# Optimization experiments

Measured on AMD Instinct MI355X. Metric: run time of the kernel, lower is better.

Reference implementation:

```python
import jax, jax.numpy as jnp
import numpy as np

UPDATE_RATE = 0.5
ALIVE_THRESH = 0.1

_SHIFTS = [(di, dj) for di in (-1, 0, 1) for dj in (-1, 0, 1) if not (di == 0 and dj == 0)]

def _laplacian(x):
    # circular 3x3 Laplacian: 8*center - 8 neighbors (wrap-around == circular pad)
    s = x * 8.0
    for di, dj in _SHIFTS:
        s = s - jnp.roll(x, (di, dj), axis=(2, 3))
    return s

def _alive_mask(alpha):
    # max_pool2d(3, stride=1) over circularly padded alpha == max over 3x3 wrap neighborhood
    m = alpha
    for di, dj in _SHIFTS:
        m = jnp.maximum(m, jnp.roll(alpha, (di, dj), axis=(2, 3)))
    return (m > ALIVE_THRESH).astype(alpha.dtype)

def setup_inputs() -> dict:
    key = jax.random.key(0)
    k1, k2, k3, k4, k5 = jax.random.split(key, 5)
    B, CHN, H, W = 4, 16, 512, 512
    PERC_N, HID = 2 * CHN, 192
    x = jax.random.uniform(k1, (B, CHN, H, W), dtype=jnp.float32)
    noise = jax.random.uniform(k2, (B, 1, H, W), dtype=jnp.float32)
    w1_w = jax.random.normal(k3, (HID, PERC_N), dtype=jnp.float32) * 0.1
    w1_b = jax.random.normal(k4, (HID,), dtype=jnp.float32) * 0.1
    w2_w = jax.random.normal(k5, (CHN, HID), dtype=jnp.float32) * 0.1
    return {"x": x, "noise": noise, "w1_w": w1_w, "w1_b": w1_b, "w2_w": w2_w}

def reference(x, noise, w1_w, w1_b, w2_w):
    alive = _alive_mask(x[:, 3:4])                       # [B,1,H,W]
    y = jnp.concatenate([x, _laplacian(x)], axis=1)      # [B,2C,H,W] perception
    h = jax.nn.relu(jnp.einsum('bchw,oc->bohw', y, w1_w) + w1_b[None, :, None, None])
    dx = jnp.einsum('bchw,oc->bohw', h, w2_w)            # [B,C,H,W]
    update_mask = jnp.floor(noise + UPDATE_RATE)         # stochastic per-pixel gate
    return (x + dx * update_mask) * alive
```

## Files before the change

### kernel.cpp

```cpp
#include <hip/hip_runtime.h>


#define HH 512
#define WW 512
#define CC 16
#define HID 192
#define NT 16
#define HW (HH * WW)

typedef _Float16 half8  __attribute__((ext_vector_type(8)));
typedef _Float16 half2v __attribute__((ext_vector_type(2)));
typedef __fp16   fp16x2 __attribute__((ext_vector_type(2)));
typedef float    f32x4  __attribute__((ext_vector_type(4)));

__device__ __forceinline__ int h2i(half2v v) { return __builtin_bit_cast(int, v); }
__device__ __forceinline__ half2v i2h(int v) { return __builtin_bit_cast(half2v, v); }

__global__ __launch_bounds__(256, 2) void nca_mfma_kernel(
    const float* __restrict__ x,
    const float* __restrict__ noise,
    const float* __restrict__ w1w,
    const float* __restrict__ w1b,
    const float* __restrict__ w2w,
    float* __restrict__ out)
{
    __shared__ __align__(16) float bl[HID];
    const int tid  = threadIdx.x;
    const int lane = tid & 63;
    const int wid  = tid >> 6;
    const int p    = lane & 15;
    const int gq   = lane >> 4;

    const int bid = blockIdx.x;
    const int lin = (bid & 7) * 128 + (bid >> 3);
    const int gr  = lin * 4 + wid;
    const int b   = gr >> 10;
    const int rem = gr & 1023;
    const int i   = rem >> 1;
    const int s   = rem & 1;
    const int start = s * (WW / 2);

    for (int k = tid; k < HID; k += 256) bl[k] = w1b[k];
    __syncthreads();

    half8 w1f[12];
    #pragma unroll
    for (int t = 0; t < 12; ++t) {
        const float* src = w1w + (16 * t + p) * 32 + 8 * gq;
        #pragma unroll
        for (int e = 0; e < 8; ++e) w1f[t][e] = (_Float16)src[e];
    }
    half8 w2f[6];
    #pragma unroll
    for (int f = 0; f < 6; ++f) {
        const float* s0 = w2w + p * HID + 32 * f + 4 * gq;
        #pragma unroll
        for (int e = 0; e < 4; ++e) {
            w2f[f][e]     = (_Float16)s0[e];
            w2f[f][4 + e] = (_Float16)s0[16 + e];
        }
    }

    const int im = (i == 0) ? HH - 1 : i - 1;
    const int ip = (i == HH - 1) ? 0 : i + 1;
    const float* xb  = x + (size_t)b * CC * HW;
    const int    cb  = 8 * (gq & 1);
    const float* xcb = xb + (size_t)cb * HW;
    const int rT = im * WW, rM = i * WW, rB = ip * WW;

    auto loadRaw = [&](int col, float r[24]) {
        #pragma unroll
        for (int e = 0; e < 8; ++e) {
            const float* pe = xcb + (size_t)e * HW;
            r[3 * e + 0] = pe[rT + col];
            r[3 * e + 1] = pe[rM + col];
            r[3 * e + 2] = pe[rB + col];
        }
    };
    auto combine = [&](const float r[24], half2v pcs[4], half2v pm[4], float& cm) {
        #pragma unroll
        for (int w = 0; w < 4; ++w) {
            const float cs0 = r[6 * w + 0] + r[6 * w + 1] + r[6 * w + 2];
            const float cs1 = r[6 * w + 3] + r[6 * w + 4] + r[6 * w + 5];
            pcs[w] = half2v{(_Float16)cs0, (_Float16)cs1};
            pm[w]  = half2v{(_Float16)r[6 * w + 1], (_Float16)r[6 * w + 4]};
        }
        cm = fmaxf(fmaxf(r[9], r[10]), r[11]);
    };

    half2v pcsA[4], pcsB[4], pcsC[4], pmB[4], pmC[4];
    float  cmA, cmB, cmC;
    float  rr[24];

    {
        float rh[24]; half2v dum[4];
        loadRaw((start - 1) & (WW - 1), rh);
        combine(rh, pcsA, dum, cmA);
        float r0[24];
        loadRaw(start + p, r0);
        combine(r0, pcsB, pmB, cmB);
        float r1[24];
        loadRaw(start + 16 + p, r1);
        combine(r1, pcsC, pmC, cmC);
    }

    const float* nrow = noise + (size_t)b * HW + rM;
    float* ob = out + (size_t)b * CC * HW;
    const f32x4* blv = (const f32x4*)bl;
    const half2v k9 = {(_Float16)9.0f, (_Float16)9.0f};
    const bool isCenter = (gq < 2);

    #pragma unroll 1
    for (int t = 0; t < NT; ++t) {
        loadRaw((start + 16 * (t + 2) + p) & (WW - 1), rr);

        union { half8 v; int iw[4]; } yf;
        #pragma unroll
        for (int w = 0; w < 4; ++w) {
            const int bw = h2i(pcsB[w]);
            int lft = __shfl_up(bw, 1, 64);
            const int patL = __shfl(h2i(pcsA[w]), lane | 15, 64);
            if (p == 0) lft = patL;
            int rgt = __shfl_down(bw, 1, 64);
            const int patR = __shfl(h2i(pcsC[w]), lane & 48, 64);
            if (p == 15) rgt = patR;
            const half2v s9  = i2h(lft) + pcsB[w] + i2h(rgt);
            const half2v lap = k9 * pmB[w] - s9;
            yf.iw[w] = isCenter ? h2i(pmB[w]) : h2i(lap);
        }

        float ml = __shfl_up(cmB, 1, 64);
        const float pml = __shfl(cmA, lane | 15, 64);
        if (p == 0) ml = pml;
        float mr = __shfl_down(cmB, 1, 64);
        const float pmr = __shfl(cmC, lane & 48, 64);
        if (p == 15) mr = pmr;
        const float rmax  = fmaxf(fmaxf(ml, cmB), mr);
        const float av    = __shfl(rmax, lane & 15, 64);
        const float alive = (av > 0.1f) ? 1.0f : 0.0f;

        const int col = start + 16 * t + p;
        const float nz = nrow[col];
        const float um = floorf(nz + 0.5f);

        f32x4 acc2a = {0.f, 0.f, 0.f, 0.f}, acc2b = {0.f, 0.f, 0.f, 0.f};
        #pragma unroll
        for (int f = 0; f < 6; ++f) {
            const f32x4 ba = blv[8 * f + gq];
            const f32x4 bb = blv[8 * f + 4 + gq];
            const f32x4 a1 = __builtin_amdgcn_mfma_f32_16x16x32_f16(w1f[2 * f],     yf.v, ba, 0, 0, 0);
            const f32x4 a2 = __builtin_amdgcn_mfma_f32_16x16x32_f16(w1f[2 * f + 1], yf.v, bb, 0, 0, 0);
            union { half8 v; fp16x2 f2[4]; } hf;
            hf.f2[0] = __builtin_amdgcn_cvt_pkrtz(fmaxf(a1[0], 0.f), fmaxf(a1[1], 0.f));
            hf.f2[1] = __builtin_amdgcn_cvt_pkrtz(fmaxf(a1[2], 0.f), fmaxf(a1[3], 0.f));
            hf.f2[2] = __builtin_amdgcn_cvt_pkrtz(fmaxf(a2[0], 0.f), fmaxf(a2[1], 0.f));
            hf.f2[3] = __builtin_amdgcn_cvt_pkrtz(fmaxf(a2[2], 0.f), fmaxf(a2[3], 0.f));
            if (f & 1) acc2b = __builtin_amdgcn_mfma_f32_16x16x32_f16(w2f[f], hf.v, acc2b, 0, 0, 0);
            else       acc2a = __builtin_amdgcn_mfma_f32_16x16x32_f16(w2f[f], hf.v, acc2a, 0, 0, 0);
        }

        #pragma unroll
        for (int r = 0; r < 4; ++r) {
            const size_t off = (size_t)(4 * gq + r) * HW + (size_t)rM + col;
            const float dx = acc2a[r] + acc2b[r];
            ob[off] = (xb[off] + dx * um) * alive;
        }

        half2v pcsD[4], pmD[4]; float cmD;
        combine(rr, pcsD, pmD, cmD);
        #pragma unroll
        for (int w = 0; w < 4; ++w) {
            pcsA[w] = pcsB[w];
            pcsB[w] = pcsC[w]; pmB[w] = pmC[w];
            pcsC[w] = pcsD[w]; pmC[w] = pmD[w];
        }
        cmA = cmB; cmB = cmC; cmC = cmD;
    }
}

extern "C" void kernel_launch(void* const* d_in, const int* in_sizes, int n_in,
                              void* d_out, int out_size, void* d_ws, size_t ws_size,
                              hipStream_t stream)
{
    const float* x     = (const float*)d_in[0];
    const float* noise = (const float*)d_in[1];
    const float* w1w   = (const float*)d_in[2];
    const float* w1b   = (const float*)d_in[3];
    const float* w2w   = (const float*)d_in[4];
    float* out = (float*)d_out;

    nca_mfma_kernel<<<1024, 256, 0, stream>>>(x, noise, w1w, w1b, w2w, out);
}
```

Measured before the change: 67.40 us.

## Reuse register-held center values for residual and prefetch noise two tiles ahead

Permutes the w2 output rows so that each lane's MFMA output channels match the center-row x values it already holds in registers. The residual add can then use those registers instead of re-reading x from global memory in the epilogue. The noise value is also prefetched two tiles ahead alongside the x loads, which keeps the load off the critical path. This adds a few more registers per thread (mx buffers and noise), which could affect occupancy at launch bounds of 2.

```diff
diff --git a/kernel.cpp b/kernel.cpp
--- a/kernel.cpp
+++ b/kernel.cpp
@@ -50,10 +50,11 @@
         #pragma unroll
         for (int e = 0; e < 8; ++e) w1f[t][e] = (_Float16)src[e];
     }
+    const int pi_p = (p & 3) | ((p & 4) << 1) | ((p & 8) >> 1);
     half8 w2f[6];
     #pragma unroll
     for (int f = 0; f < 6; ++f) {
-        const float* s0 = w2w + p * HID + 32 * f + 4 * gq;
+        const float* s0 = w2w + pi_p * HID + 32 * f + 4 * gq;
         #pragma unroll
         for (int e = 0; e < 4; ++e) {
             w2f[f][e]     = (_Float16)s0[e];
@@ -67,6 +68,8 @@
     const int    cb  = 8 * (gq & 1);
     const float* xcb = xb + (size_t)cb * HW;
     const int rT = im * WW, rM = i * WW, rB = ip * WW;
+    const int eSel = 4 * (gq >> 1);
+    const int gqsw = ((gq & 1) << 1) | (gq >> 1);
 
     auto loadRaw = [&](int col, float r[24]) {
         #pragma unroll
@@ -77,7 +80,8 @@
             r[3 * e + 2] = pe[rB + col];
         }
     };
-    auto combine = [&](const float r[24], half2v pcs[4], half2v pm[4], float& cm) {
+    auto combine = [&](const float r[24], half2v pcs[4], half2v pm[4],
+                       float mx[4], float& cm) {
         #pragma unroll
         for (int w = 0; w < 4; ++w) {
             const float cs0 = r[6 * w + 0] + r[6 * w + 1] + r[6 * w + 2];
@@ -85,26 +89,33 @@
             pcs[w] = half2v{(_Float16)cs0, (_Float16)cs1};
             pm[w]  = half2v{(_Float16)r[6 * w + 1], (_Float16)r[6 * w + 4]};
         }
+        #pragma unroll
+        for (int j = 0; j < 4; ++j) mx[j] = r[3 * (eSel + j) + 1];
         cm = fmaxf(fmaxf(r[9], r[10]), r[11]);
     };
 
     half2v pcsA[4], pcsB[4], pcsC[4], pmB[4], pmC[4];
+    float  mxB[4], mxC[4];
     float  cmA, cmB, cmC;
+    float  nzB, nzC;
     float  rr[24];
 
+    const float* nrow = noise + (size_t)b * HW + rM;
+
     {
-        float rh[24]; half2v dum[4];
+        float rh[24]; half2v dum[4]; float dmx[4];
         loadRaw((start - 1) & (WW - 1), rh);
-        combine(rh, pcsA, dum, cmA);
+        combine(rh, pcsA, dum, dmx, cmA);
         float r0[24];
         loadRaw(start + p, r0);
-        combine(r0, pcsB, pmB, cmB);
+        combine(r0, pcsB, pmB, mxB, cmB);
         float r1[24];
         loadRaw(start + 16 + p, r1);
-        combine(r1, pcsC, pmC, cmC);
-    }
-
-    const float* nrow = noise + (size_t)b * HW + rM;
+        combine(r1, pcsC, pmC, mxC, cmC);
+        nzB = nrow[start + p];
+        nzC = nrow[start + 16 + p];
+    }
+
     float* ob = out + (size_t)b * CC * HW;
     const f32x4* blv = (const f32x4*)bl;
     const half2v k9 = {(_Float16)9.0f, (_Float16)9.0f};
@@ -112,7 +123,9 @@
 
     #pragma unroll 1
     for (int t = 0; t < NT; ++t) {
-        loadRaw((start + 16 * (t + 2) + p) & (WW - 1), rr);
+        const int colP = (start + 16 * (t + 2) + p) & (WW - 1);
+        loadRaw(colP, rr);
+        const float nzD = nrow[colP];
 
         union { half8 v; int iw[4]; } yf;
         #pragma unroll
@@ -138,10 +151,7 @@
         const float rmax  = fmaxf(fmaxf(ml, cmB), mr);
         const float av    = __shfl(rmax, lane & 15, 64);
         const float alive = (av > 0.1f) ? 1.0f : 0.0f;
-
-        const int col = start + 16 * t + p;
-        const float nz = nrow[col];
-        const float um = floorf(nz + 0.5f);
+        const float um    = floorf(nzB + 0.5f);
 
         f32x4 acc2a = {0.f, 0.f, 0.f, 0.f}, acc2b = {0.f, 0.f, 0.f, 0.f};
         #pragma unroll
@@ -159,22 +169,26 @@
             else       acc2a = __builtin_amdgcn_mfma_f32_16x16x32_f16(w2f[f], hf.v, acc2a, 0, 0, 0);
         }
 
+        const int col = start + 16 * t + p;
         #pragma unroll
         for (int r = 0; r < 4; ++r) {
-            const size_t off = (size_t)(4 * gq + r) * HW + (size_t)rM + col;
+            const size_t off = (size_t)(4 * gqsw + r) * HW + (size_t)rM + col;
             const float dx = acc2a[r] + acc2b[r];
-            ob[off] = (xb[off] + dx * um) * alive;
-        }
-
-        half2v pcsD[4], pmD[4]; float cmD;
-        combine(rr, pcsD, pmD, cmD);
+            ob[off] = (mxB[r] + dx * um) * alive;
+        }
+
+        half2v pcsD[4], pmD[4]; float mxD[4]; float cmD;
+        combine(rr, pcsD, pmD, mxD, cmD);
         #pragma unroll
         for (int w = 0; w < 4; ++w) {
             pcsA[w] = pcsB[w];
             pcsB[w] = pcsC[w]; pmB[w] = pmC[w];
             pcsC[w] = pcsD[w]; pmC[w] = pmD[w];
         }
+        #pragma unroll
+        for (int j = 0; j < 4; ++j) { mxB[j] = mxC[j]; mxC[j] = mxD[j]; }
         cmA = cmB; cmB = cmC; cmC = cmD;
+        nzB = nzC; nzC = nzD;
     }
 }
 
```

After: 89.49 us. 1.33x slower.
